# Kernel optimization log

Hardware: AMD Instinct MI355X
Metric: run time of the kernel (lower is better)

## Reference

```python
import jax, jax.numpy as jnp
import numpy as np

B, Q, P = 4, 512, 512
Q_SIZE, P_SIZE, V_SIZE = 512, 512, 256


def setup_inputs() -> dict:
    key = jax.random.key(0)
    k1, k2, k3, k4, k5 = jax.random.split(key, 5)
    hq = jax.random.normal(k1, (B, Q, Q_SIZE), dtype=jnp.float32)
    hp = jax.random.normal(k2, (B, P, P_SIZE), dtype=jnp.float32)
    # Linear weights stored as [in, out] for x @ W; scaled like default init
    W1 = jax.random.normal(k3, (Q_SIZE, V_SIZE), dtype=jnp.float32) / np.sqrt(Q_SIZE)
    W2 = jax.random.normal(k4, (P_SIZE, V_SIZE), dtype=jnp.float32) / np.sqrt(P_SIZE)
    v = jax.random.normal(k5, (V_SIZE,), dtype=jnp.float32) / np.sqrt(V_SIZE)
    return {"hq": hq, "hp": hp, "W1": W1, "W2": W2, "v": v}


def reference(hq, hp, W1, W2, v):
    # Projections: [B,Q,V], [B,P,V]
    sq = jnp.einsum("bqd,dv->bqv", hq, W1)
    sp = jnp.einsum("bpe,ev->bpv", hp, W2)
    # Additive (Bahdanau) scores: broadcast add -> tanh -> dot with v: [B,P,Q]
    s = jnp.einsum("bpqv,v->bpq", jnp.tanh(sp[:, :, None, :] + sq[:, None, :, :]), v)
    # softmax over Q (dim=2 after squeeze), then weighted sum over hq: [B,P,q_size]
    a = jax.nn.softmax(s, axis=2)
    return jnp.einsum("bpq,bqd->bpd", a, hq)
```

## Files before the change

kernel.cpp:

```cpp
#include <hip/hip_runtime.h>

#define VDIM 256
#define DDIM 512
#define LOG2E     1.4426950408889634f
#define TWO_LOG2E 2.8853900817779268f

typedef float  f32x4   __attribute__((ext_vector_type(4)));
typedef short  short8v __attribute__((ext_vector_type(8)));

__device__ __forceinline__ unsigned short f2bf(float f) {
    unsigned int u = __float_as_uint(f);
    u += 0x7fffu + ((u >> 16) & 1u);
    return (unsigned short)(u >> 16);
}
__device__ __forceinline__ float bf2f(unsigned short b) {
    return __uint_as_float(((unsigned int)b) << 16);
}

__device__ __forceinline__ void split4(const float4 f, uint2* hi, uint2* lo) {
    const unsigned u0 = __float_as_uint(f.x), u1 = __float_as_uint(f.y);
    const unsigned u2 = __float_as_uint(f.z), u3 = __float_as_uint(f.w);
    const unsigned h0 = u0 & 0xFFFF0000u, h1 = u1 & 0xFFFF0000u;
    const unsigned h2 = u2 & 0xFFFF0000u, h3 = u3 & 0xFFFF0000u;
    hi->x = (u0 >> 16) | h1;
    hi->y = (u2 >> 16) | h3;
    const float l0 = f.x - __uint_as_float(h0), l1 = f.y - __uint_as_float(h1);
    const float l2 = f.z - __uint_as_float(h2), l3 = f.w - __uint_as_float(h3);
    lo->x = (__float_as_uint(l0) >> 16) | (__float_as_uint(l1) & 0xFFFF0000u);
    lo->y = (__float_as_uint(l2) >> 16) | (__float_as_uint(l3) & 0xFFFF0000u);
}

__global__ __launch_bounds__(256) void transpose_conv(
    const float* __restrict__ hq,
    const float* __restrict__ W1, const float* __restrict__ W2,
    ushort* __restrict__ hqT_hi, ushort* __restrict__ hqT_lo,
    ushort* __restrict__ W1T_hi, ushort* __restrict__ W1T_lo,
    ushort* __restrict__ W2T_hi, ushort* __restrict__ W2T_lo)
{
    const int z = blockIdx.z;
    const float* src; ushort *dhi, *dlo;
    int ld_src, ld_dst, src_cols;
    if (z < 4)      { src = hq + ((size_t)z << 18); dhi = hqT_hi + ((size_t)z << 18);
                      dlo = hqT_lo + ((size_t)z << 18); ld_src = 512; ld_dst = 512; src_cols = 512; }
    else if (z == 4){ src = W1; dhi = W1T_hi; dlo = W1T_lo; ld_src = 256; ld_dst = 512; src_cols = 256; }
    else            { src = W2; dhi = W2T_hi; dlo = W2T_lo; ld_src = 256; ld_dst = 512; src_cols = 256; }

    const int r0 = blockIdx.y << 6, c0 = blockIdx.x << 6;
    if (c0 >= src_cols) return;

    __shared__ float tile[64][65];
    const int t = threadIdx.x;
    #pragma unroll
    for (int i = 0; i < 4; ++i) {
        const int r = (i << 4) + (t >> 4);
        const int c = (t & 15) << 2;
        const float4 v = *(const float4*)(src + (size_t)(r0 + r) * ld_src + c0 + c);
        tile[r][c + 0] = v.x; tile[r][c + 1] = v.y;
        tile[r][c + 2] = v.z; tile[r][c + 3] = v.w;
    }
    __syncthreads();
    #pragma unroll
    for (int i = 0; i < 4; ++i) {
        const int a  = (i << 4) + (t >> 4);
        const int bb = (t & 15) << 2;
        ushort4 hi, lo;
        float f;
        f = tile[bb + 0][a]; hi.x = f2bf(f); lo.x = f2bf(f - bf2f(hi.x));
        f = tile[bb + 1][a]; hi.y = f2bf(f); lo.y = f2bf(f - bf2f(hi.y));
        f = tile[bb + 2][a]; hi.z = f2bf(f); lo.z = f2bf(f - bf2f(hi.z));
        f = tile[bb + 3][a]; hi.w = f2bf(f); lo.w = f2bf(f - bf2f(hi.w));
        const size_t o = (size_t)(c0 + a) * ld_dst + r0 + bb;
        *(ushort4*)(dhi + o) = hi;
        *(ushort4*)(dlo + o) = lo;
    }
}

#define SWZ(r, c) (((r) << 8) + ((c) ^ (((r) & 15) << 4)))

__global__ __launch_bounds__(256) void proj_mfma(
    const float* __restrict__ hq, const float* __restrict__ hp,
    const ushort* __restrict__ W1T_hi, const ushort* __restrict__ W1T_lo,
    const ushort* __restrict__ W2T_hi, const ushort* __restrict__ W2T_lo,
    float* __restrict__ EqT, float* __restrict__ Ep)
{
    const int by = blockIdx.y;
    const bool isQ = by < 32;
    const int m0 = (by & 31) << 6;
    const int n0 = blockIdx.x << 6;
    const float*  __restrict__ A   = isQ ? hq : hp;
    const ushort* __restrict__ Bhi = isQ ? W1T_hi : W2T_hi;
    const ushort* __restrict__ Blo = isQ ? W1T_lo : W2T_lo;

    __shared__ __attribute__((aligned(16))) ushort As[64 * 128];
    __shared__ __attribute__((aligned(16))) ushort Bs[64 * 128];
    char* AsB = (char*)As;
    char* BsB = (char*)Bs;

    const int t = threadIdx.x;
    const int w = t >> 6, l = t & 63;
    const int moff = (w & 1) << 5, noff = (w >> 1) << 5;

    f32x4 acc[2][2];
    #pragma unroll
    for (int i = 0; i < 2; ++i)
        #pragma unroll
        for (int j = 0; j < 2; ++j)
            acc[i][j] = (f32x4){0.f, 0.f, 0.f, 0.f};

    const int sr = t >> 2;
    const int sc = t & 3;
    const size_t argA = (size_t)(m0 + sr) * 512;
    const size_t argB = (size_t)(n0 + sr) * 512;

    for (int k0 = 0; k0 < 512; k0 += 64) {
        const float4 f0 = *(const float4*)(A + argA + k0 + (sc << 4) + 0);
        const float4 f1 = *(const float4*)(A + argA + k0 + (sc << 4) + 4);
        const float4 f2 = *(const float4*)(A + argA + k0 + (sc << 4) + 8);
        const float4 f3 = *(const float4*)(A + argA + k0 + (sc << 4) + 12);
        const uint4 b0 = *(const uint4*)(Bhi + argB + k0 + (sc << 4));
        const uint4 b1 = *(const uint4*)(Bhi + argB + k0 + (sc << 4) + 8);
        const uint4 b2 = *(const uint4*)(Blo + argB + k0 + (sc << 4));
        const uint4 b3 = *(const uint4*)(Blo + argB + k0 + (sc << 4) + 8);

        uint4 ah0, al0, ah1, al1;
        split4(f0, (uint2*)&ah0.x, (uint2*)&al0.x);
        split4(f1, (uint2*)&ah0.z, (uint2*)&al0.z);
        split4(f2, (uint2*)&ah1.x, (uint2*)&al1.x);
        split4(f3, (uint2*)&ah1.z, (uint2*)&al1.z);

        __syncthreads();
        *(uint4*)(AsB + SWZ(sr, (sc << 5)))            = ah0;
        *(uint4*)(AsB + SWZ(sr, (sc << 5) + 16))       = ah1;
        *(uint4*)(AsB + SWZ(sr, 128 + (sc << 5)))      = al0;
        *(uint4*)(AsB + SWZ(sr, 128 + (sc << 5) + 16)) = al1;
        *(uint4*)(BsB + SWZ(sr, (sc << 5)))            = b0;
        *(uint4*)(BsB + SWZ(sr, (sc << 5) + 16))       = b1;
        *(uint4*)(BsB + SWZ(sr, 128 + (sc << 5)))      = b2;
        *(uint4*)(BsB + SWZ(sr, 128 + (sc << 5) + 16)) = b3;
        __syncthreads();

        #pragma unroll
        for (int kc = 0; kc < 2; ++kc) {
            const int colh = (kc << 6) + ((l >> 4) << 4);
            short8v ahi[2], alo[2], bhi[2], blo[2];
            #pragma unroll
            for (int mt = 0; mt < 2; ++mt) {
                const int r = moff + (mt << 4) + (l & 15);
                ahi[mt] = *(const short8v*)(AsB + SWZ(r, colh));
                alo[mt] = *(const short8v*)(AsB + SWZ(r, colh + 128));
            }
            #pragma unroll
            for (int nt = 0; nt < 2; ++nt) {
                const int r = noff + (nt << 4) + (l & 15);
                bhi[nt] = *(const short8v*)(BsB + SWZ(r, colh));
                blo[nt] = *(const short8v*)(BsB + SWZ(r, colh + 128));
            }
            #pragma unroll
            for (int mt = 0; mt < 2; ++mt)
                #pragma unroll
                for (int nt = 0; nt < 2; ++nt) {
                    acc[mt][nt] = __builtin_amdgcn_mfma_f32_16x16x32_bf16(ahi[mt], bhi[nt], acc[mt][nt], 0, 0, 0);
                    acc[mt][nt] = __builtin_amdgcn_mfma_f32_16x16x32_bf16(ahi[mt], blo[nt], acc[mt][nt], 0, 0, 0);
                    acc[mt][nt] = __builtin_amdgcn_mfma_f32_16x16x32_bf16(alo[mt], bhi[nt], acc[mt][nt], 0, 0, 0);
                }
        }
    }

    #pragma unroll
    for (int mt = 0; mt < 2; ++mt)
        #pragma unroll
        for (int nt = 0; nt < 2; ++nt)
            #pragma unroll
            for (int r = 0; r < 4; ++r) {
                const int row = m0 + moff + (mt << 4) + ((l >> 4) << 2) + r;
                const int col = n0 + noff + (nt << 4) + (l & 15);
                const float e = __builtin_amdgcn_exp2f(acc[mt][nt][r] * TWO_LOG2E);
                if (isQ) {
                    const int bb = row >> 9, q = row & 511;
                    EqT[((((size_t)bb << 6) + (col >> 2)) * 512 + q) * 4 + (col & 3)] = e;
                } else {
                    Ep[(size_t)row * VDIM + col] = e;
                }
            }
}

__global__ __launch_bounds__(256) void out_mfma(
    const ushort* __restrict__ Ahi, const ushort* __restrict__ Alo,
    const ushort* __restrict__ Bhi_, const ushort* __restrict__ Blo_,
    float* __restrict__ C)
{
    const int m0 = blockIdx.y << 6;
    const int n0 = blockIdx.x << 6;
    const size_t off = (size_t)(m0 >> 9) << 18;
    const ushort* __restrict__ Bhi = Bhi_ + off;
    const ushort* __restrict__ Blo = Blo_ + off;

    __shared__ __attribute__((aligned(16))) ushort As[64 * 128];
    __shared__ __attribute__((aligned(16))) ushort Bs[64 * 128];
    char* AsB = (char*)As;
    char* BsB = (char*)Bs;

    const int t = threadIdx.x;
    const int w = t >> 6, l = t & 63;
    const int moff = (w & 1) << 5, noff = (w >> 1) << 5;

    f32x4 acc[2][2];
    #pragma unroll
    for (int i = 0; i < 2; ++i)
        #pragma unroll
        for (int j = 0; j < 2; ++j)
            acc[i][j] = (f32x4){0.f, 0.f, 0.f, 0.f};

    const int sr = t >> 2;
    const int sc = t & 3;
    const size_t argA = (size_t)(m0 + sr) * 512;
    const size_t argB = (size_t)(n0 + sr) * 512;

    for (int k0 = 0; k0 < 512; k0 += 64) {
        const uint4 a0 = *(const uint4*)(Ahi + argA + k0 + (sc << 4));
        const uint4 a1 = *(const uint4*)(Ahi + argA + k0 + (sc << 4) + 8);
        const uint4 a2 = *(const uint4*)(Alo + argA + k0 + (sc << 4));
        const uint4 a3 = *(const uint4*)(Alo + argA + k0 + (sc << 4) + 8);
        const uint4 b0 = *(const uint4*)(Bhi + argB + k0 + (sc << 4));
        const uint4 b1 = *(const uint4*)(Bhi + argB + k0 + (sc << 4) + 8);
        const uint4 b2 = *(const uint4*)(Blo + argB + k0 + (sc << 4));
        const uint4 b3 = *(const uint4*)(Blo + argB + k0 + (sc << 4) + 8);
        __syncthreads();
        *(uint4*)(AsB + SWZ(sr, (sc << 5)))            = a0;
        *(uint4*)(AsB + SWZ(sr, (sc << 5) + 16))       = a1;
        *(uint4*)(AsB + SWZ(sr, 128 + (sc << 5)))      = a2;
        *(uint4*)(AsB + SWZ(sr, 128 + (sc << 5) + 16)) = a3;
        *(uint4*)(BsB + SWZ(sr, (sc << 5)))            = b0;
        *(uint4*)(BsB + SWZ(sr, (sc << 5) + 16))       = b1;
        *(uint4*)(BsB + SWZ(sr, 128 + (sc << 5)))      = b2;
        *(uint4*)(BsB + SWZ(sr, 128 + (sc << 5) + 16)) = b3;
        __syncthreads();
        #pragma unroll
        for (int kc = 0; kc < 2; ++kc) {
            const int colh = (kc << 6) + ((l >> 4) << 4);
            short8v ahi[2], alo[2], bhi[2], blo[2];
            #pragma unroll
            for (int mt = 0; mt < 2; ++mt) {
                const int r = moff + (mt << 4) + (l & 15);
                ahi[mt] = *(const short8v*)(AsB + SWZ(r, colh));
                alo[mt] = *(const short8v*)(AsB + SWZ(r, colh + 128));
            }
            #pragma unroll
            for (int nt = 0; nt < 2; ++nt) {
                const int r = noff + (nt << 4) + (l & 15);
                bhi[nt] = *(const short8v*)(BsB + SWZ(r, colh));
                blo[nt] = *(const short8v*)(BsB + SWZ(r, colh + 128));
            }
            #pragma unroll
            for (int mt = 0; mt < 2; ++mt)
                #pragma unroll
                for (int nt = 0; nt < 2; ++nt) {
                    acc[mt][nt] = __builtin_amdgcn_mfma_f32_16x16x32_bf16(ahi[mt], bhi[nt], acc[mt][nt], 0, 0, 0);
                    acc[mt][nt] = __builtin_amdgcn_mfma_f32_16x16x32_bf16(ahi[mt], blo[nt], acc[mt][nt], 0, 0, 0);
                    acc[mt][nt] = __builtin_amdgcn_mfma_f32_16x16x32_bf16(alo[mt], bhi[nt], acc[mt][nt], 0, 0, 0);
                }
        }
    }

    #pragma unroll
    for (int mt = 0; mt < 2; ++mt)
        #pragma unroll
        for (int nt = 0; nt < 2; ++nt)
            #pragma unroll
            for (int r = 0; r < 4; ++r) {
                const int row = m0 + moff + (mt << 4) + ((l >> 4) << 2) + r;
                const int col = n0 + noff + (nt << 4) + (l & 15);
                C[(size_t)row * 512 + col] = acc[mt][nt][r];
            }
}

template<bool FUSED>
__global__ __launch_bounds__(512) void score_softmax(
    const float4* __restrict__ EqT, const float* __restrict__ Ep,
    const float* __restrict__ vvec, const float* __restrict__ hq,
    ushort* __restrict__ a_hi, ushort* __restrict__ a_lo,
    float* __restrict__ out)
{
    const int blk = blockIdx.x;
    const int b   = blk >> 7;
    const int p0  = (blk & 127) << 2;

    __shared__ __attribute__((aligned(16))) float score[4][512];
    const int t = threadIdx.x;

    const float4* __restrict__ wv = (const float4*)vvec;
    const float4* __restrict__ eq = EqT + ((size_t)b << 15) + t;
    const float*  epb             = Ep + (size_t)((b << 9) + p0) * VDIM;

    float a0 = 0.f, a1 = 0.f, a2 = 0.f, a3 = 0.f;

    #pragma unroll 4
    for (int vi = 0; vi < 64; ++vi) {
        const float4 e = eq[vi << 9];
        const float4 w = wv[vi];
#define ROWTERM(i, accv) { \
        const float4 p = *((const float4*)(epb + (i) * VDIM) + vi); \
        const float t0 = fmaf(p.x, e.x, 1.f), t1 = fmaf(p.y, e.y, 1.f); \
        const float t2 = fmaf(p.z, e.z, 1.f), t3 = fmaf(p.w, e.w, 1.f); \
        const float d01 = t0 * t1, d23 = t2 * t3, den = d01 * d23; \
        const float n01 = fmaf(w.x, t1, w.y * t0); \
        const float n23 = fmaf(w.z, t3, w.w * t2); \
        const float num = fmaf(n01, d23, n23 * d01); \
        accv = fmaf(num, __builtin_amdgcn_rcpf(den), accv); }
        ROWTERM(0, a0) ROWTERM(1, a1) ROWTERM(2, a2) ROWTERM(3, a3)
#undef ROWTERM
    }
    score[0][t] = a0; score[1][t] = a1; score[2][t] = a2; score[3][t] = a3;
    __syncthreads();

    {
        const int wid = t >> 6, lane = t & 63;
        if (wid < 4) {
            float vals[8];
            float m = -1e30f;
            #pragma unroll
            for (int i = 0; i < 8; ++i) {
                vals[i] = -2.f * score[wid][lane + (i << 6)];
                m = fmaxf(m, vals[i]);
            }
            #pragma unroll
            for (int off = 32; off; off >>= 1) m = fmaxf(m, __shfl_xor(m, off));
            float sum = 0.f;
            #pragma unroll
            for (int i = 0; i < 8; ++i) {
                vals[i] = __builtin_amdgcn_exp2f((vals[i] - m) * LOG2E);
                sum += vals[i];
            }
            #pragma unroll
            for (int off = 32; off; off >>= 1) sum += __shfl_xor(sum, off);
            const float inv = __builtin_amdgcn_rcpf(sum);
            #pragma unroll
            for (int i = 0; i < 8; ++i) score[wid][lane + (i << 6)] = vals[i] * inv;
        }
    }
    __syncthreads();

    if (!FUSED) {
        #pragma unroll
        for (int r = 0; r < 4; ++r) {
            const float f = score[r][t];
            const ushort h  = f2bf(f);
            const ushort lo = f2bf(f - bf2f(h));
            a_hi[(size_t)((b << 9) + p0 + r) * 512 + t] = h;
            a_lo[(size_t)((b << 9) + p0 + r) * 512 + t] = lo;
        }
    } else {
        float ax[4] = {};
        #pragma unroll 4
        for (int q = 0; q < 512; ++q) {
            const float h = hq[(size_t)((b << 9) + q) * DDIM + t];
            #pragma unroll
            for (int r = 0; r < 4; ++r) ax[r] = fmaf(score[r][q], h, ax[r]);
        }
        #pragma unroll
        for (int r = 0; r < 4; ++r)
            out[(size_t)((b << 9) + p0 + r) * DDIM + t] = ax[r];
    }
}

__global__ __launch_bounds__(256) void proj_exp_gemm_f32(
    const float* __restrict__ hq, const float* __restrict__ hp,
    const float* __restrict__ W1, const float* __restrict__ W2,
    float* __restrict__ Eq, float* __restrict__ Ep)
{
    const int by = blockIdx.y;
    const float *A, *W;
    if (by < 64) { A = hq; W = W1; }
    else         { A = hp; W = W2; }
    const int m0 = (by & 63) * 32;
    const int n0 = blockIdx.x * 64;

    __shared__ __attribute__((aligned(16))) float As[16][36];
    __shared__ __attribute__((aligned(16))) float Bs[16][68];

    const int tid  = threadIdx.x;
    const int tr = tid >> 4, tc = tid & 15;
    const int la_r = tid >> 3, la_c = (tid & 7) << 1;
    const int lb_r = tid >> 4, lb_c = (tid & 15) << 2;

    float acc[2][4] = {};
    for (int k0 = 0; k0 < 512; k0 += 16) {
        float2 a2 = *(const float2*)(A + (size_t)(m0 + la_r) * 512 + k0 + la_c);
        float4 b4 = *(const float4*)(W + (size_t)(k0 + lb_r) * VDIM + n0 + lb_c);
        __syncthreads();
        As[la_c + 0][la_r] = a2.x;
        As[la_c + 1][la_r] = a2.y;
        *(float4*)&Bs[lb_r][lb_c] = b4;
        __syncthreads();
        #pragma unroll
        for (int kk = 0; kk < 16; ++kk) {
            float2 av = *(const float2*)&As[kk][tr << 1];
            float4 bv = *(const float4*)&Bs[kk][tc << 2];
            const float* ap = (const float*)&av;
            const float* bp = (const float*)&bv;
            #pragma unroll
            for (int i = 0; i < 2; ++i)
                #pragma unroll
                for (int j = 0; j < 4; ++j)
                    acc[i][j] = fmaf(ap[i], bp[j], acc[i][j]);
        }
    }
    if (by < 64) {
        float4* EqT = (float4*)Eq;
        const int bb = m0 >> 9, qb = m0 & 511;
        const int vi = (blockIdx.x << 4) + tc;
        #pragma unroll
        for (int i = 0; i < 2; ++i) {
            float4 r;
            r.x = __builtin_amdgcn_exp2f(acc[i][0] * TWO_LOG2E);
            r.y = __builtin_amdgcn_exp2f(acc[i][1] * TWO_LOG2E);
            r.z = __builtin_amdgcn_exp2f(acc[i][2] * TWO_LOG2E);
            r.w = __builtin_amdgcn_exp2f(acc[i][3] * TWO_LOG2E);
            EqT[((size_t)(bb << 6) + vi) * 512 + qb + (tr << 1) + i] = r;
        }
    } else {
        #pragma unroll
        for (int i = 0; i < 2; ++i) {
            float4 r;
            r.x = __builtin_amdgcn_exp2f(acc[i][0] * TWO_LOG2E);
            r.y = __builtin_amdgcn_exp2f(acc[i][1] * TWO_LOG2E);
            r.z = __builtin_amdgcn_exp2f(acc[i][2] * TWO_LOG2E);
            r.w = __builtin_amdgcn_exp2f(acc[i][3] * TWO_LOG2E);
            *(float4*)(Ep + (size_t)(m0 + (tr << 1) + i) * VDIM + n0 + (tc << 2)) = r;
        }
    }
}

extern "C" void kernel_launch(void* const* d_in, const int* in_sizes, int n_in,
                              void* d_out, int out_size, void* d_ws, size_t ws_size,
                              hipStream_t stream)
{
    const float* hq = (const float*)d_in[0];
    const float* hp = (const float*)d_in[1];
    const float* W1 = (const float*)d_in[2];
    const float* W2 = (const float*)d_in[3];
    const float* vv = (const float*)d_in[4];
    float* out = (float*)d_out;

    float* EqT = (float*)d_ws;
    float* Ep  = EqT + 524288;
    ushort* u  = (ushort*)(Ep + 524288);
    ushort* hqT_hi = u; u += 1048576;
    ushort* hqT_lo = u; u += 1048576;
    ushort* W1T_hi = u; u += 131072;
    ushort* W1T_lo = u; u += 131072;
    ushort* W2T_hi = u; u += 131072;
    ushort* W2T_lo = u; u += 131072;
    ushort* a_hi   = u; u += 1048576;
    ushort* a_lo   = u; u += 1048576;
    const size_t need = (size_t)((char*)u - (char*)d_ws);

    if (ws_size >= need) {
        transpose_conv<<<dim3(8, 8, 6), 256, 0, stream>>>(
            hq, W1, W2, hqT_hi, hqT_lo, W1T_hi, W1T_lo, W2T_hi, W2T_lo);
        proj_mfma<<<dim3(4, 64), 256, 0, stream>>>(
            hq, hp, W1T_hi, W1T_lo, W2T_hi, W2T_lo, EqT, Ep);
        score_softmax<false><<<512, 512, 0, stream>>>(
            (const float4*)EqT, Ep, vv, hq, a_hi, a_lo, out);
        out_mfma<<<dim3(8, 32), 256, 0, stream>>>(a_hi, a_lo, hqT_hi, hqT_lo, out);
    } else {
        proj_exp_gemm_f32<<<dim3(4, 128), 256, 0, stream>>>(hq, hp, W1, W2, EqT, Ep);
        score_softmax<true><<<512, 512, 0, stream>>>(
            (const float4*)EqT, Ep, vv, hq, nullptr, nullptr, out);
    }
}
```

Measured before the change: 58.64 us.

## Overlap hq transpose with projection GEMM and prefetch EqT in score loop

Moves the hq transpose and bf16 split out of the first kernel and into extra blocks of the projection kernel. The prologue kernel now only handles the small weight matrices, and the hq transpose runs alongside the GEMM blocks instead of on the critical path before them. Shared memory is unified into one buffer reused by both block roles. The score loop also software-prefetches the next EqT vector into a register, which costs extra register pressure.

New measurement: 58.53 us. No clear change (-0.2%).

```diff
diff --git a/kernel.cpp b/kernel.cpp
--- a/kernel.cpp
+++ b/kernel.cpp
@@ -30,23 +30,15 @@
     lo->y = (__float_as_uint(l2) >> 16) | (__float_as_uint(l3) & 0xFFFF0000u);
 }
 
-__global__ __launch_bounds__(256) void transpose_conv(
-    const float* __restrict__ hq,
+__global__ __launch_bounds__(256) void w_transpose(
     const float* __restrict__ W1, const float* __restrict__ W2,
-    ushort* __restrict__ hqT_hi, ushort* __restrict__ hqT_lo,
     ushort* __restrict__ W1T_hi, ushort* __restrict__ W1T_lo,
     ushort* __restrict__ W2T_hi, ushort* __restrict__ W2T_lo)
 {
-    const int z = blockIdx.z;
-    const float* src; ushort *dhi, *dlo;
-    int ld_src, ld_dst, src_cols;
-    if (z < 4)      { src = hq + ((size_t)z << 18); dhi = hqT_hi + ((size_t)z << 18);
-                      dlo = hqT_lo + ((size_t)z << 18); ld_src = 512; ld_dst = 512; src_cols = 512; }
-    else if (z == 4){ src = W1; dhi = W1T_hi; dlo = W1T_lo; ld_src = 256; ld_dst = 512; src_cols = 256; }
-    else            { src = W2; dhi = W2T_hi; dlo = W2T_lo; ld_src = 256; ld_dst = 512; src_cols = 256; }
-
+    const float* src = blockIdx.z ? W2 : W1;
+    ushort* dhi = blockIdx.z ? W2T_hi : W1T_hi;
+    ushort* dlo = blockIdx.z ? W2T_lo : W1T_lo;
     const int r0 = blockIdx.y << 6, c0 = blockIdx.x << 6;
-    if (c0 >= src_cols) return;
 
     __shared__ float tile[64][65];
     const int t = threadIdx.x;
@@ -54,7 +46,7 @@
     for (int i = 0; i < 4; ++i) {
         const int r = (i << 4) + (t >> 4);
         const int c = (t & 15) << 2;
-        const float4 v = *(const float4*)(src + (size_t)(r0 + r) * ld_src + c0 + c);
+        const float4 v = *(const float4*)(src + (size_t)(r0 + r) * 256 + c0 + c);
         tile[r][c + 0] = v.x; tile[r][c + 1] = v.y;
         tile[r][c + 2] = v.z; tile[r][c + 3] = v.w;
     }
@@ -69,7 +61,7 @@
         f = tile[bb + 1][a]; hi.y = f2bf(f); lo.y = f2bf(f - bf2f(hi.y));
         f = tile[bb + 2][a]; hi.z = f2bf(f); lo.z = f2bf(f - bf2f(hi.z));
         f = tile[bb + 3][a]; hi.w = f2bf(f); lo.w = f2bf(f - bf2f(hi.w));
-        const size_t o = (size_t)(c0 + a) * ld_dst + r0 + bb;
+        const size_t o = (size_t)(c0 + a) * 512 + r0 + bb;
         *(ushort4*)(dhi + o) = hi;
         *(ushort4*)(dlo + o) = lo;
     }
@@ -77,26 +69,62 @@
 
 #define SWZ(r, c) (((r) << 8) + ((c) ^ (((r) & 15) << 4)))
 
-__global__ __launch_bounds__(256) void proj_mfma(
+__global__ __launch_bounds__(256) void proj_and_transpose(
     const float* __restrict__ hq, const float* __restrict__ hp,
     const ushort* __restrict__ W1T_hi, const ushort* __restrict__ W1T_lo,
     const ushort* __restrict__ W2T_hi, const ushort* __restrict__ W2T_lo,
+    ushort* __restrict__ hqT_hi, ushort* __restrict__ hqT_lo,
     float* __restrict__ EqT, float* __restrict__ Ep)
 {
-    const int by = blockIdx.y;
+    __shared__ __attribute__((aligned(16))) char smem[32768];
+    const int bid = blockIdx.x;
+    const int t = threadIdx.x;
+
+    if (bid >= 256) {
+        const int k  = bid - 256;
+        const int z  = k >> 6;
+        const int r0 = ((k >> 3) & 7) << 6, c0 = (k & 7) << 6;
+        const float* src = hq + ((size_t)z << 18);
+        ushort* dhi = hqT_hi + ((size_t)z << 18);
+        ushort* dlo = hqT_lo + ((size_t)z << 18);
+        float (*tile)[65] = (float(*)[65])smem;
+        #pragma unroll
+        for (int i = 0; i < 4; ++i) {
+            const int r = (i << 4) + (t >> 4);
+            const int c = (t & 15) << 2;
+            const float4 v = *(const float4*)(src + (size_t)(r0 + r) * 512 + c0 + c);
+            tile[r][c + 0] = v.x; tile[r][c + 1] = v.y;
+            tile[r][c + 2] = v.z; tile[r][c + 3] = v.w;
+        }
+        __syncthreads();
+        #pragma unroll
+        for (int i = 0; i < 4; ++i) {
+            const int a  = (i << 4) + (t >> 4);
+            const int bb = (t & 15) << 2;
+            ushort4 hi, lo;
+            float f;
+            f = tile[bb + 0][a]; hi.x = f2bf(f); lo.x = f2bf(f - bf2f(hi.x));
+            f = tile[bb + 1][a]; hi.y = f2bf(f); lo.y = f2bf(f - bf2f(hi.y));
+            f = tile[bb + 2][a]; hi.z = f2bf(f); lo.z = f2bf(f - bf2f(hi.z));
+            f = tile[bb + 3][a]; hi.w = f2bf(f); lo.w = f2bf(f - bf2f(hi.w));
+            const size_t o = (size_t)(c0 + a) * 512 + r0 + bb;
+            *(ushort4*)(dhi + o) = hi;
+            *(ushort4*)(dlo + o) = lo;
+        }
+        return;
+    }
+
+    const int by = bid >> 2;
     const bool isQ = by < 32;
     const int m0 = (by & 31) << 6;
-    const int n0 = blockIdx.x << 6;
+    const int n0 = (bid & 3) << 6;
     const float*  __restrict__ A   = isQ ? hq : hp;
     const ushort* __restrict__ Bhi = isQ ? W1T_hi : W2T_hi;
     const ushort* __restrict__ Blo = isQ ? W1T_lo : W2T_lo;
 
-    __shared__ __attribute__((aligned(16))) ushort As[64 * 128];
-    __shared__ __attribute__((aligned(16))) ushort Bs[64 * 128];
-    char* AsB = (char*)As;
-    char* BsB = (char*)Bs;
-
-    const int t = threadIdx.x;
+    char* AsB = smem;
+    char* BsB = smem + 16384;
+
     const int w = t >> 6, l = t & 63;
     const int moff = (w & 1) << 5, noff = (w >> 1) << 5;
 
@@ -289,19 +317,21 @@
     const int t = threadIdx.x;
 
     const float4* __restrict__ wv = (const float4*)vvec;
-    const float4* __restrict__ eq = EqT + ((size_t)b << 15) + t;
-    const float*  epb             = Ep + (size_t)((b << 9) + p0) * VDIM;
+    const float4* __restrict__ eqp = EqT + ((size_t)b << 15) + t;
+    const float*  epb              = Ep + (size_t)((b << 9) + p0) * VDIM;
 
     float a0 = 0.f, a1 = 0.f, a2 = 0.f, a3 = 0.f;
+    float4 e = eqp[0];
 
     #pragma unroll 4
     for (int vi = 0; vi < 64; ++vi) {
-        const float4 e = eq[vi << 9];
+        const float4 ec = e;
+        if (vi < 63) e = eqp[(vi + 1) << 9];
         const float4 w = wv[vi];
 #define ROWTERM(i, accv) { \
         const float4 p = *((const float4*)(epb + (i) * VDIM) + vi); \
-        const float t0 = fmaf(p.x, e.x, 1.f), t1 = fmaf(p.y, e.y, 1.f); \
-        const float t2 = fmaf(p.z, e.z, 1.f), t3 = fmaf(p.w, e.w, 1.f); \
+        const float t0 = fmaf(p.x, ec.x, 1.f), t1 = fmaf(p.y, ec.y, 1.f); \
+        const float t2 = fmaf(p.z, ec.z, 1.f), t3 = fmaf(p.w, ec.w, 1.f); \
         const float d01 = t0 * t1, d23 = t2 * t3, den = d01 * d23; \
         const float n01 = fmaf(w.x, t1, w.y * t0); \
         const float n23 = fmaf(w.z, t3, w.w * t2); \
@@ -456,10 +486,10 @@
     const size_t need = (size_t)((char*)u - (char*)d_ws);
 
     if (ws_size >= need) {
-        transpose_conv<<<dim3(8, 8, 6), 256, 0, stream>>>(
-            hq, W1, W2, hqT_hi, hqT_lo, W1T_hi, W1T_lo, W2T_hi, W2T_lo);
-        proj_mfma<<<dim3(4, 64), 256, 0, stream>>>(
-            hq, hp, W1T_hi, W1T_lo, W2T_hi, W2T_lo, EqT, Ep);
+        w_transpose<<<dim3(4, 8, 2), 256, 0, stream>>>(
+            W1, W2, W1T_hi, W1T_lo, W2T_hi, W2T_lo);
+        proj_and_transpose<<<512, 256, 0, stream>>>(
+            hq, hp, W1T_hi, W1T_lo, W2T_hi, W2T_lo, hqT_hi, hqT_lo, EqT, Ep);
         score_softmax<false><<<512, 512, 0, stream>>>(
             (const float4*)EqT, Ep, vv, hq, a_hi, a_lo, out);
         out_mfma<<<dim3(8, 32), 256, 0, stream>>>(a_hi, a_lo, hqT_hi, hqT_lo, out);
```
